# Kernel optimization log

Measured on AMD Instinct MI355X. Metric: run time of the kernel, lower is better.

The kernel has to match this reference:

```python
import jax, jax.numpy as jnp
import numpy as np

B, C, HID, H, W = 32, 256, 128, 32, 32  # batch, input_dim, hidden_dim, grid


def conv1x1(x, Wt, b):
    # 1x1 Conv2d == channel-mixing matmul. x: [B,Cin,H,W], Wt: [Cout,Cin]
    return jnp.einsum('oc,bchw->bohw', Wt, x) + b[None, :, None, None]


def setup_inputs() -> dict:
    key = jax.random.key(0)
    ks = jax.random.split(key, 18)
    p = lambda k, shape: (jax.random.normal(k, shape, jnp.float32) * 0.02)
    return {
        'h': jax.random.normal(ks[0], (B, C, H, W), jnp.float32),
        'm': jax.random.normal(ks[1], (B, C, H, W), jnp.float32),
        'Wq': p(ks[2], (HID, C)),  'bq': p(ks[3], (HID,)),
        'Wk': p(ks[4], (HID, C)),  'bk': p(ks[5], (HID,)),
        'Wv': p(ks[6], (C, C)),    'bv': p(ks[7], (C,)),
        'Wk2': p(ks[8], (HID, C)), 'bk2': p(ks[9], (HID,)),
        'Wv2': p(ks[10], (C, C)),  'bv2': p(ks[11], (C,)),
        'Wz': p(ks[12], (2 * C, 2 * C)), 'bz': p(ks[13], (2 * C,)),
        'Wm': p(ks[14], (3 * C, 3 * C)), 'bm': p(ks[15], (3 * C,)),
    }


def reference(h, m, Wq, bq, Wk, bk, Wv, bv, Wk2, bk2, Wv2, bv2, Wz, bz, Wm, bm):
    Bb, Cc, Hh, Ww = h.shape
    HW = Hh * Ww
    # shared query from h: [B, HID, HW]
    q = conv1x1(h, Wq, bq).reshape(Bb, -1, HW)
    # self-attention branch over h (unscaled logits, as in original)
    kh = conv1x1(h, Wk, bk).reshape(Bb, -1, HW)
    A_h = jax.nn.softmax(jnp.einsum('bdp,bdq->bpq', q, kh), axis=-1)  # [B,HW,HW]
    vh = conv1x1(h, Wv, bv).reshape(Bb, Cc, HW)
    Z_h = jnp.einsum('bpq,bcq->bcp', A_h, vh).reshape(Bb, Cc, Hh, Ww)
    # cross-attention branch over memory m with shared q
    km = conv1x1(m, Wk2, bk2).reshape(Bb, -1, HW)
    A_m = jax.nn.softmax(jnp.einsum('bdp,bdq->bpq', q, km), axis=-1)
    vm = conv1x1(m, Wv2, bv2).reshape(Bb, Cc, HW)
    Z_m = jnp.einsum('bpq,bcq->bcp', A_m, vm).reshape(Bb, Cc, Hh, Ww)
    # fuse, then LSTM-style gating
    Z = conv1x1(jnp.concatenate([Z_h, Z_m], axis=1), Wz, bz)          # [B,2C,H,W]
    comb = conv1x1(jnp.concatenate([Z, h], axis=1), Wm, bm)           # [B,3C,H,W]
    mo, mg, mi = jnp.split(comb, 3, axis=1)
    mi = jax.nn.sigmoid(mi)
    new_m = (1.0 - mi) * m + mi * jnp.tanh(mg)
    new_h = jax.nn.sigmoid(mo) * new_m
    return new_h, new_m
```

## Files before the change

kernel.cpp:

```cpp
#include <hip/hip_runtime.h>
#include <hip/hip_bf16.h>

typedef __bf16  v8bf __attribute__((ext_vector_type(8)));
typedef float   v4f  __attribute__((ext_vector_type(4)));
typedef float   f4   __attribute__((ext_vector_type(4)));
typedef unsigned short us8 __attribute__((ext_vector_type(8)));
typedef unsigned short us4 __attribute__((ext_vector_type(4)));
typedef unsigned int u32;

#define BATCH 32
#define CDIM  256
#define HW    1024

#define OFF_HBT 0L
#define OFF_MBT (OFF_HBT + 16777216L)
#define OFF_QKH (OFF_MBT + 16777216L)
#define OFF_QKM (OFF_QKH + 16777216L)
#define OFF_VH  (OFF_QKM + 8388608L)
#define OFF_VM  (OFF_VH  + 16777216L)
#define OFF_ZCT (OFF_VM  + 16777216L)
#define OFF_W   (OFF_ZCT + 33554432L)
#define OFF_B   (OFF_W   + 3866624L)
#define OFF_CMB OFF_MBT
#define WS_TOTAL (OFF_B + 2944L * 4)
#define W_QK  0
#define W_K2  65536
#define W_V   98304
#define W_V2  163840
#define W_M   491520
#define W_ZT  1081344
#define W_F   1343488
#define B_QK  0
#define B_K2  256
#define B_V   384
#define B_V2  640
#define B_F   2176

__device__ inline unsigned short f2u(float x) {
    __hip_bfloat16 h = __float2bfloat16(x);
    union { __hip_bfloat16 h; unsigned short u; } cv; cv.h = h; return cv.u;
}
__device__ inline float u2f(unsigned short u) {
    union { unsigned short u; __hip_bfloat16 h; } cv; cv.u = u; return __bfloat162float(cv.h);
}
__device__ inline float sigmoidf_(float x) {
    x = fminf(fmaxf(x, -30.f), 30.f);
    return 1.f / (1.f + __expf(-x));
}
__device__ inline float tanhf_(float x) {
    x = fminf(fmaxf(x, -15.f), 15.f);
    float e = __expf(2.f * x);
    return (e - 1.f) / (e + 1.f);
}
__device__ inline void glds16(const unsigned short* g, unsigned short* l) {
    __builtin_amdgcn_global_load_lds(
        (const __attribute__((address_space(1))) u32*)g,
        (__attribute__((address_space(3))) u32*)l, 16, 0, 0);
}

__global__ __launch_bounds__(256)
void prep(const float* __restrict__ hsrc, const float* __restrict__ msrc,
          const float* __restrict__ Wq, const float* __restrict__ Wk,
          const float* __restrict__ Wv, const float* __restrict__ Wk2,
          const float* __restrict__ Wv2, const float* __restrict__ Wz,
          const float* __restrict__ Wm,
          const float* __restrict__ bq, const float* __restrict__ bk,
          const float* __restrict__ bk2, const float* __restrict__ bv,
          const float* __restrict__ bv2, const float* __restrict__ bz,
          const float* __restrict__ bm,
          char* __restrict__ ws)
{
    __shared__ float t[64][68];
    unsigned short* wdst = (unsigned short*)(ws + OFF_W);
    float*          bdst = (float*)(ws + OFF_B);
    const int bid = blockIdx.x;
    const int tid = threadIdx.x;

    if (bid < 6025) {
        const int gid = bid * 256 + tid;
        if (gid < 1081344) {
            const float* s; int off;
            if      (gid <   32768) { s = Wq;  off = gid; }
            else if (gid <   65536) { s = Wk;  off = gid -   32768; }
            else if (gid <   98304) { s = Wk2; off = gid -   65536; }
            else if (gid <  163840) { s = Wv;  off = gid -   98304; }
            else if (gid <  229376) { s = Wv2; off = gid -  163840; }
            else if (gid <  491520) { s = Wz;  off = gid -  229376; }
            else                    { s = Wm;  off = gid -  491520; }
            wdst[gid] = f2u(s[off]);
        } else if (gid < 1343488) {
            const int idx = gid - 1081344;
            const int k = idx >> 9, j = idx & 511;
            wdst[gid] = f2u(Wz[j * 512 + k]);
        } else if (gid < 1540096) {
            const int idx = gid - 1343488;
            const int o = idx >> 8, kk = 512 + (idx & 255);
            wdst[W_F + o * 768 + kk] = f2u(Wm[o * 768 + kk]);
        } else {
            const int bi = gid - 1540096;
            if (bi < 2176) {
                const float* s; int off;
                if      (bi <  128) { s = bq;  off = bi; }
                else if (bi <  256) { s = bk;  off = bi -  128; }
                else if (bi <  384) { s = bk2; off = bi -  256; }
                else if (bi <  640) { s = bv;  off = bi -  384; }
                else if (bi <  896) { s = bv2; off = bi -  640; }
                else if (bi < 1408) { s = bz;  off = bi -  896; }
                else                { s = bm;  off = bi - 1408; }
                bdst[bi] = s[off];
            }
        }
    } else if (bid < 6028) {
        const int o = (bid - 6025) * 256 + tid;
        if (o < 768) {
            float s = bm[o];
            const float* r = Wm + (long)o * 768;
#pragma unroll 8
            for (int j = 0; j < 512; ++j) s += r[j] * bz[j];
            bdst[B_F + o] = s;
        }
    } else {
        const int tz = bid - 6028;
        const int z  = tz >> 6;
        const int p0 = (tz & 15) * 64;
        const int c0 = ((tz >> 4) & 3) * 64;
        const float* src = (z < BATCH) ? hsrc + (long)z * CDIM * HW
                                       : msrc + (long)(z - BATCH) * CDIM * HW;
        unsigned short* dst = (unsigned short*)(ws + ((z < BATCH) ? OFF_HBT : OFF_MBT))
                              + (long)((z < BATCH) ? z : z - BATCH) * HW * CDIM;
        const int r  = tid >> 4;
        const int c4 = (tid & 15) * 4;
#pragma unroll
        for (int i = 0; i < 4; ++i) {
            const f4 v = *reinterpret_cast<const f4*>(src + (long)(c0 + r + 16 * i) * HW + p0 + c4);
            t[r + 16 * i][c4 + 0] = v[0];
            t[r + 16 * i][c4 + 1] = v[1];
            t[r + 16 * i][c4 + 2] = v[2];
            t[r + 16 * i][c4 + 3] = v[3];
        }
        __syncthreads();
#pragma unroll
        for (int i = 0; i < 4; ++i) {
            const int pr = r + 16 * i;
            us4 o;
#pragma unroll
            for (int j = 0; j < 4; ++j) o[j] = f2u(t[c4 + j][pr]);
            *reinterpret_cast<us4*>(dst + (long)(p0 + pr) * CDIM + c0 + c4) = o;
        }
    }
}

__device__ __forceinline__
void gemm_core(const unsigned short* __restrict__ A, int lda,
               const unsigned short* __restrict__ A2, int lda2, int kswitch,
               const unsigned short* __restrict__ Bt, int ldb,
               unsigned short* __restrict__ Cp, int ldc,
               int K, const float* __restrict__ bias, int biasMode,
               int m0, int n0,
               unsigned short* As, unsigned short* Bs)
{
    const int tid  = threadIdx.x;
    const int lane = tid & 63;
    const int w    = tid >> 6;

    v4f acc[4][4];
#pragma unroll
    for (int i = 0; i < 4; ++i)
#pragma unroll
        for (int j = 0; j < 4; ++j) acc[i][j] = v4f{0.f, 0.f, 0.f, 0.f};

    const int wm   = (w >> 1) * 64;
    const int wn   = (w & 1) * 64;
    const int fr   = lane & 15;
    const int g    = lane >> 4;

    const int arow = (w << 3) + (lane >> 3);
    const int acol = (((lane & 7) ^ ((lane >> 3) & 7)) * 8);
    const int lbase = (w << 9);

    for (int k0 = 0; k0 < K; k0 += 64) {
        const unsigned short* Ab; int Al; int Ao;
        if (k0 < kswitch) { Ab = A;  Al = lda;  Ao = k0; }
        else              { Ab = A2; Al = lda2; Ao = k0 - kswitch; }
        const unsigned short* ga = Ab + (long)(m0 + arow) * Al + Ao + acol;
        const unsigned short* gb = Bt + (long)(n0 + arow) * ldb + k0 + acol;
#pragma unroll
        for (int i = 0; i < 4; ++i) {
            glds16(ga + (long)(32 * i) * Al, &As[i * 2048 + lbase]);
            glds16(gb + (long)(32 * i) * ldb, &Bs[i * 2048 + lbase]);
        }
        __syncthreads();
#pragma unroll
        for (int ks = 0; ks < 2; ++ks) {
            const int slot = ((ks * 4 + g) ^ (fr & 7)) * 8;
            v8bf af[4], bfv[4];
#pragma unroll
            for (int mi = 0; mi < 4; ++mi)
                af[mi] = *reinterpret_cast<const v8bf*>(&As[(wm + mi * 16 + fr) * 64 + slot]);
#pragma unroll
            for (int ni = 0; ni < 4; ++ni)
                bfv[ni] = *reinterpret_cast<const v8bf*>(&Bs[(wn + ni * 16 + fr) * 64 + slot]);
#pragma unroll
            for (int mi = 0; mi < 4; ++mi)
#pragma unroll
                for (int ni = 0; ni < 4; ++ni)
                    acc[mi][ni] = __builtin_amdgcn_mfma_f32_16x16x32_bf16(af[mi], bfv[ni], acc[mi][ni], 0, 0, 0);
        }
        __syncthreads();
    }

    const int rbase0 = m0 + wm + g * 4;
#pragma unroll
    for (int mi = 0; mi < 4; ++mi) {
#pragma unroll
        for (int ni = 0; ni < 4; ++ni) {
            const int col = n0 + wn + ni * 16 + fr;
            const int rb  = rbase0 + mi * 16;
            const float bn = (biasMode == 1) ? bias[col] : 0.f;
#pragma unroll
            for (int r = 0; r < 4; ++r) {
                float x = acc[mi][ni][r] + bn;
                if (biasMode == 2) x += bias[rb + r];
                Cp[(long)(rb + r) * ldc + col] = f2u(x);
            }
        }
    }
}

__global__ __launch_bounds__(256)
void gemm_multi(char* __restrict__ ws)
{
    __shared__ unsigned short As[128 * 64];
    __shared__ unsigned short Bs[128 * 64];
    unsigned short* wA = (unsigned short*)(ws + OFF_W);
    float*          bA = (float*)(ws + OFF_B);
    const int id = blockIdx.x;

    if (id < 512) {
        const int b = id >> 4, x = id & 7, y = (id >> 3) & 1;
        const unsigned short* A = (unsigned short*)(ws + OFF_HBT) + (long)b * 262144;
        gemm_core(A, 256, A, 256, 1 << 30, wA + W_QK, 256,
                  (unsigned short*)(ws + OFF_QKH) + (long)b * 262144, 256,
                  256, bA + B_QK, 1, x * 128, y * 128, As, Bs);
    } else if (id < 768) {
        const int idx = id - 512, b = idx >> 3, x = idx & 7;
        const unsigned short* A = (unsigned short*)(ws + OFF_MBT) + (long)b * 262144;
        gemm_core(A, 256, A, 256, 1 << 30, wA + W_K2, 256,
                  (unsigned short*)(ws + OFF_QKM) + (long)b * 131072, 128,
                  256, bA + B_K2, 1, x * 128, 0, As, Bs);
    } else if (id < 1280) {
        const int idx = id - 768, b = idx >> 4, x = idx & 1, y = (idx >> 1) & 7;
        gemm_core(wA + W_V, 256, wA + W_V, 256, 1 << 30,
                  (unsigned short*)(ws + OFF_HBT) + (long)b * 262144, 256,
                  (unsigned short*)(ws + OFF_VH) + (long)b * 262144, 1024,
                  256, bA + B_V, 2, x * 128, y * 128, As, Bs);
    } else if (id < 1792) {
        const int idx = id - 1280, b = idx >> 4, x = idx & 1, y = (idx >> 1) & 7;
        gemm_core(wA + W_V2, 256, wA + W_V2, 256, 1 << 30,
                  (unsigned short*)(ws + OFF_MBT) + (long)b * 262144, 256,
                  (unsigned short*)(ws + OFF_VM) + (long)b * 262144, 1024,
                  256, bA + B_V2, 2, x * 128, y * 128, As, Bs);
    } else {
        const int idx = id - 1792, x = idx % 6, y = idx / 6;
        gemm_core(wA + W_M, 768, wA + W_M, 768, 1 << 30, wA + W_ZT, 512,
                  wA + W_F, 768, 512, bA, 0, x * 128, y * 128, As, Bs);
    }
}

__global__ __launch_bounds__(256)
void gemm_bf16(const unsigned short* __restrict__ A, int lda, long sA,
               const unsigned short* __restrict__ A2, int lda2, long sA2, int kswitch,
               const unsigned short* __restrict__ Bt, int ldb, long sB,
               unsigned short* __restrict__ Cp, int ldc, long sC,
               int K, const float* __restrict__ bias, int biasMode)
{
    __shared__ unsigned short As[128 * 64];
    __shared__ unsigned short Bs[128 * 64];
    const int b = blockIdx.z;
    gemm_core(A + (long)b * sA, lda, A2 + (long)b * sA2, lda2, kswitch,
              Bt + (long)b * sB, ldb, Cp + (long)b * sC, ldc,
              K, bias, biasMode, blockIdx.x * 128, blockIdx.y * 128, As, Bs);
}

__global__ __launch_bounds__(512, 4)
void attn_fused(const unsigned short* __restrict__ Qb, long sQ, int ldq,
                const unsigned short* __restrict__ K0, long sK0, int ldk0,
                const unsigned short* __restrict__ V0,
                const unsigned short* __restrict__ K1, long sK1, int ldk1,
                const unsigned short* __restrict__ V1,
                unsigned short* __restrict__ Out, long sO)
{
    __shared__ unsigned short Qs[64 * 128];
    __shared__ unsigned short Ks[64 * 128];
    __shared__ unsigned short Vs[256 * 64];
    __shared__ unsigned short Ps[64 * 64];

    const int id = blockIdx.x;
    const int c8 = id & 7;
    const int k  = id >> 3;
    const int z  = c8 * 8 + (k >> 4);
    const int p0 = (k & 15) * 64;

    const int b  = (z < 32) ? z : z - 32;
    const unsigned short* Kp; const unsigned short* Vp; int ldk, outoff;
    if (z < 32) { Kp = K0 + (long)b * sK0; Vp = V0 + (long)b * 262144L; ldk = ldk0; outoff = 0; }
    else        { Kp = K1 + (long)b * sK1; Vp = V1 + (long)b * 262144L; ldk = ldk1; outoff = 256; }
    const unsigned short* Qp = Qb + (long)b * sQ;
    Out += (long)b * sO;

    const int tid  = threadIdx.x;
    const int lane = tid & 63;
    const int w    = tid >> 6;
    const int fr   = lane & 15;
    const int g    = lane >> 4;
    const int wp   = w >> 2;
    const int wq   = w & 3;

    v4f vacc[2][4];
#pragma unroll
    for (int i = 0; i < 2; ++i)
#pragma unroll
        for (int j = 0; j < 4; ++j) vacc[i][j] = v4f{0.f, 0.f, 0.f, 0.f};
    float rp[2][4];
#pragma unroll
    for (int i = 0; i < 2; ++i)
#pragma unroll
        for (int r = 0; r < 4; ++r) rp[i][r] = 0.f;

    const int srow   = tid >> 4;
    const int schunk = ((tid & 15) ^ (srow & 7)) * 8;
    const int vrow   = tid >> 3;
    const int vchunk = ((tid & 7) ^ (vrow & 7)) * 8;
    const int sdst   = w * 512;
    const int kr     = wq * 16 + fr;

#define TSWZ(p) (((p) & 7) ^ ((((p) >> 3) & 1) * 3))

#define STAGE_Q()                                                              \
    { _Pragma("unroll")                                                        \
      for (int i = 0; i < 2; ++i)                                              \
          glds16(Qp + (long)(p0 + i * 32 + srow) * ldq + schunk,               \
                 &Qs[i * 4096 + sdst]); }
#define STAGE_K(t)                                                             \
    { const int kv0 = (t) * 64;                                                \
      _Pragma("unroll")                                                        \
      for (int i = 0; i < 2; ++i)                                              \
          glds16(Kp + (long)(kv0 + i * 32 + srow) * ldk + schunk,              \
                 &Ks[i * 4096 + sdst]); }
#define STAGE_V(t)                                                             \
    { const int kv0 = (t) * 64;                                                \
      _Pragma("unroll")                                                        \
      for (int i = 0; i < 4; ++i)                                              \
          glds16(Vp + (long)(i * 64 + vrow) * 1024 + kv0 + vchunk,             \
                 &Vs[i * 4096 + sdst]); }

    STAGE_Q();
    STAGE_K(0);

    for (int t = 0; t < 16; ++t) {
        __syncthreads();
        STAGE_V(t);

        v4f sacc[2];
#pragma unroll
        for (int mi = 0; mi < 2; ++mi) sacc[mi] = v4f{0.f, 0.f, 0.f, 0.f};
        __builtin_amdgcn_s_setprio(1);
#pragma unroll
        for (int ks = 0; ks < 4; ++ks) {
            const v8bf kf = *reinterpret_cast<const v8bf*>(
                &Ks[kr * 128 + ((ks * 4 + g) ^ (kr & 7)) * 8]);
#pragma unroll
            for (int mi = 0; mi < 2; ++mi) {
                const int qrow = wp * 32 + mi * 16 + fr;
                const v8bf qf = *reinterpret_cast<const v8bf*>(
                    &Qs[qrow * 128 + ((ks * 4 + g) ^ (qrow & 7)) * 8]);
                sacc[mi] = __builtin_amdgcn_mfma_f32_16x16x32_bf16(qf, kf, sacc[mi], 0, 0, 0);
            }
        }
        __builtin_amdgcn_s_setprio(0);
#pragma unroll
        for (int mi = 0; mi < 2; ++mi)
#pragma unroll
            for (int r = 0; r < 4; ++r) {
                const float e = __expf(sacc[mi][r]);
                rp[mi][r] += e;
                const int prow = wp * 32 + mi * 16 + g * 4 + r;
                Ps[prow * 64 + (kr ^ (TSWZ(prow) << 3))] = f2u(e);
            }

        __syncthreads();
        if (t < 15) STAGE_K(t + 1);

        __builtin_amdgcn_s_setprio(1);
#pragma unroll
        for (int ks = 0; ks < 2; ++ks) {
            v8bf pf[2], vf[4];
#pragma unroll
            for (int mi = 0; mi < 2; ++mi) {
                const int pr = wp * 32 + mi * 16 + fr;
                pf[mi] = *reinterpret_cast<const v8bf*>(
                    &Ps[pr * 64 + ((ks * 4 + g) ^ TSWZ(pr)) * 8]);
            }
#pragma unroll
            for (int ni = 0; ni < 4; ++ni) {
                const int vr = wq * 64 + ni * 16 + fr;
                vf[ni] = *reinterpret_cast<const v8bf*>(
                    &Vs[vr * 64 + ((ks * 4 + g) ^ (vr & 7)) * 8]);
            }
#pragma unroll
            for (int mi = 0; mi < 2; ++mi)
#pragma unroll
                for (int ni = 0; ni < 4; ++ni)
                    vacc[mi][ni] = __builtin_amdgcn_mfma_f32_16x16x32_bf16(pf[mi], vf[ni], vacc[mi][ni], 0, 0, 0);
        }
        __builtin_amdgcn_s_setprio(0);
    }
#undef STAGE_Q
#undef STAGE_K
#undef STAGE_V
#undef TSWZ

    __syncthreads();
    float* red = reinterpret_cast<float*>(Ps);
#pragma unroll
    for (int mi = 0; mi < 2; ++mi)
#pragma unroll
        for (int r = 0; r < 4; ++r) {
            float v = rp[mi][r];
            v += __shfl_xor(v, 1);
            v += __shfl_xor(v, 2);
            v += __shfl_xor(v, 4);
            v += __shfl_xor(v, 8);
            if (fr == 0) red[wq * 64 + wp * 32 + mi * 16 + g * 4 + r] = v;
        }
    __syncthreads();

#pragma unroll
    for (int mi = 0; mi < 2; ++mi)
#pragma unroll
        for (int r = 0; r < 4; ++r) {
            const int pl = wp * 32 + mi * 16 + g * 4 + r;
            const float inv = 1.f / (red[pl] + red[64 + pl] + red[128 + pl] + red[192 + pl]);
#pragma unroll
            for (int ni = 0; ni < 4; ++ni)
                Out[(long)(p0 + pl) * 512 + outoff + wq * 64 + ni * 16 + fr]
                    = f2u(vacc[mi][ni][r] * inv);
        }
}

__global__ __launch_bounds__(256)
void gating(const unsigned short* __restrict__ combT, const float* __restrict__ m,
            float* __restrict__ outh, float* __restrict__ outm)
{
    const int b  = blockIdx.y;
    const int p0 = blockIdx.x * 32;
    __shared__ unsigned short t[32 * 776];
    const unsigned short* src = combT + ((long)b * HW + p0) * 768;
    const int tid = threadIdx.x;
    for (int i = tid; i < 32 * 96; i += 256) {
        const int rr = i / 96;
        const int cc = (i % 96) * 8;
        *reinterpret_cast<us8*>(&t[rr * 776 + cc]) =
            *reinterpret_cast<const us8*>(src + (long)rr * 768 + cc);
    }
    __syncthreads();
    const int pl = tid & 31;
    const int cl = tid >> 5;
    for (int ci = 0; ci < 32; ++ci) {
        const int c = ci * 8 + cl;
        const float mo = u2f(t[pl * 776 + c]);
        const float mg = u2f(t[pl * 776 + 256 + c]);
        const float mi = u2f(t[pl * 776 + 512 + c]);
        const long gi = ((long)b * CDIM + c) * HW + p0 + pl;
        const float mv = m[gi];
        const float ms = sigmoidf_(mi);
        const float nm = (1.f - ms) * mv + ms * tanhf_(mg);
        const float nh = sigmoidf_(mo) * nm;
        outh[gi] = nh;
        outm[gi] = nm;
    }
}

extern "C" void kernel_launch(void* const* d_in, const int* in_sizes, int n_in,
                              void* d_out, int out_size, void* d_ws, size_t ws_size,
                              hipStream_t stream)
{
    const float* h   = (const float*)d_in[0];
    const float* m   = (const float*)d_in[1];
    const float* Wq  = (const float*)d_in[2];
    const float* bq  = (const float*)d_in[3];
    const float* Wk  = (const float*)d_in[4];
    const float* bk  = (const float*)d_in[5];
    const float* Wv  = (const float*)d_in[6];
    const float* bv  = (const float*)d_in[7];
    const float* Wk2 = (const float*)d_in[8];
    const float* bk2 = (const float*)d_in[9];
    const float* Wv2 = (const float*)d_in[10];
    const float* bv2 = (const float*)d_in[11];
    const float* Wz  = (const float*)d_in[12];
    const float* bz  = (const float*)d_in[13];
    const float* Wm  = (const float*)d_in[14];
    const float* bm  = (const float*)d_in[15];

    char* ws = (char*)d_ws;
    if (ws_size < (size_t)WS_TOTAL) return;

    unsigned short* hT  = (unsigned short*)(ws + OFF_HBT);
    unsigned short* qkh = (unsigned short*)(ws + OFF_QKH);
    unsigned short* qkm = (unsigned short*)(ws + OFF_QKM);
    unsigned short* vh  = (unsigned short*)(ws + OFF_VH);
    unsigned short* vm  = (unsigned short*)(ws + OFF_VM);
    unsigned short* zct = (unsigned short*)(ws + OFF_ZCT);
    unsigned short* cmb = (unsigned short*)(ws + OFF_CMB);
    unsigned short* wA  = (unsigned short*)(ws + OFF_W);
    float*          bA  = (float*)(ws + OFF_B);

    float* outh = (float*)d_out;
    float* outm = outh + 8388608L;

    prep<<<dim3(10124), dim3(256), 0, stream>>>(
        h, m, Wq, Wk, Wv, Wk2, Wv2, Wz, Wm,
        bq, bk, bk2, bv, bv2, bz, bm, ws);

    gemm_multi<<<dim3(1816), dim3(256), 0, stream>>>(ws);

    attn_fused<<<dim3(1024), dim3(512), 0, stream>>>(
        qkh, 262144L, 256,
        qkh + 128, 262144L, 256, vh,
        qkm, 131072L, 128, vm,
        zct, 524288L);

    gemm_bf16<<<dim3(8, 6, 32), dim3(256), 0, stream>>>(
        zct, 512, 524288L, hT, 256, 262144L, 512,
        wA + W_F, 768, 0L, cmb, 768, 786432L, 768, bA + B_F, 1);

    gating<<<dim3(32, 32), dim3(256), 0, stream>>>(cmb, m, outh, outm);
}
```

Baseline: 243.9 us.

## Replace batched comb GEMM with 256x256-tile double-buffered kernel and simplify P swizzle

The final combination GEMM moves from a batched 128x128-tile launch to a flattened-M kernel with 256x256 tiles and 512 threads. It double-buffers LDS stages with explicit vmcnt waits and barriers, and remaps workgroup IDs in an XCD-aware order. The larger tiles are meant to raise operand reuse and overlap loads with MFMA work, at the cost of more LDS and registers and a smaller grid. Separately, the attention kernel's P-tile swizzle is simplified to a plain row XOR, which may change LDS bank conflicts.

```diff
diff --git a/kernel.cpp b/kernel.cpp
--- a/kernel.cpp
+++ b/kernel.cpp
@@ -267,19 +267,107 @@
     }
 }
 
-__global__ __launch_bounds__(256)
-void gemm_bf16(const unsigned short* __restrict__ A, int lda, long sA,
-               const unsigned short* __restrict__ A2, int lda2, long sA2, int kswitch,
-               const unsigned short* __restrict__ Bt, int ldb, long sB,
-               unsigned short* __restrict__ Cp, int ldc, long sC,
-               int K, const float* __restrict__ bias, int biasMode)
+__global__ __launch_bounds__(512, 2)
+void comb_gemm(const unsigned short* __restrict__ A, int lda,
+               const unsigned short* __restrict__ A2, int lda2, int kswitch,
+               const unsigned short* __restrict__ Bt, int ldb,
+               unsigned short* __restrict__ Cp, int ldc,
+               int K, const float* __restrict__ bias, int ntilesN)
 {
-    __shared__ unsigned short As[128 * 64];
-    __shared__ unsigned short Bs[128 * 64];
-    const int b = blockIdx.z;
-    gemm_core(A + (long)b * sA, lda, A2 + (long)b * sA2, lda2, kswitch,
-              Bt + (long)b * sB, ldb, Cp + (long)b * sC, ldc,
-              K, bias, biasMode, blockIdx.x * 128, blockIdx.y * 128, As, Bs);
+    __shared__ unsigned short As[2][256 * 64];
+    __shared__ unsigned short Bs[2][256 * 64];
+
+    const int nwg = gridDim.x;
+    const int wg  = (blockIdx.x & 7) * (nwg >> 3) + (blockIdx.x >> 3);
+    const int m0  = (wg / ntilesN) * 256;
+    const int n0  = (wg % ntilesN) * 256;
+
+    const int tid  = threadIdx.x;
+    const int lane = tid & 63;
+    const int w    = tid >> 6;
+    const int fr   = lane & 15;
+    const int g    = lane >> 4;
+    const int wm   = (w >> 2) * 128;
+    const int wn   = (w & 3) * 64;
+
+    const int srow   = tid >> 3;
+    const int schunk = ((tid & 7) ^ (srow & 7)) * 8;
+    const int sdst   = w * 512;
+
+    v4f acc[8][4];
+#pragma unroll
+    for (int i = 0; i < 8; ++i)
+#pragma unroll
+        for (int j = 0; j < 4; ++j) acc[i][j] = v4f{0.f, 0.f, 0.f, 0.f};
+
+    const int nt = K >> 6;
+
+#define CSTAGE(t, bi)                                                          \
+    { const int k0 = (t) * 64;                                                 \
+      const unsigned short* Ab; int Al; int Ao;                                \
+      if (k0 < kswitch) { Ab = A;  Al = lda;  Ao = k0; }                       \
+      else              { Ab = A2; Al = lda2; Ao = k0 - kswitch; }             \
+      _Pragma("unroll")                                                        \
+      for (int i = 0; i < 4; ++i) {                                            \
+          glds16(Ab + (long)(m0 + i * 64 + srow) * Al + Ao + schunk,           \
+                 &As[bi][i * 4096 + sdst]);                                    \
+          glds16(Bt + (long)(n0 + i * 64 + srow) * ldb + k0 + schunk,          \
+                 &Bs[bi][i * 4096 + sdst]);                                    \
+      } }
+
+    CSTAGE(0, 0);
+    CSTAGE(1, 1);
+
+    for (int t = 0; t < nt; ++t) {
+        if (t + 1 < nt) asm volatile("s_waitcnt vmcnt(8)" ::: "memory");
+        else            asm volatile("s_waitcnt vmcnt(0)" ::: "memory");
+        __builtin_amdgcn_s_barrier();
+        asm volatile("" ::: "memory");
+
+        const unsigned short* Ar = As[t & 1];
+        const unsigned short* Br = Bs[t & 1];
+        __builtin_amdgcn_s_setprio(1);
+#pragma unroll
+        for (int ks = 0; ks < 2; ++ks) {
+            v8bf af[8], bf[4];
+#pragma unroll
+            for (int mi = 0; mi < 8; ++mi) {
+                const int r = wm + mi * 16 + fr;
+                af[mi] = *reinterpret_cast<const v8bf*>(
+                    &Ar[r * 64 + ((ks * 4 + g) ^ (r & 7)) * 8]);
+            }
+#pragma unroll
+            for (int ni = 0; ni < 4; ++ni) {
+                const int r = wn + ni * 16 + fr;
+                bf[ni] = *reinterpret_cast<const v8bf*>(
+                    &Br[r * 64 + ((ks * 4 + g) ^ (r & 7)) * 8]);
+            }
+#pragma unroll
+            for (int mi = 0; mi < 8; ++mi)
+#pragma unroll
+                for (int ni = 0; ni < 4; ++ni)
+                    acc[mi][ni] = __builtin_amdgcn_mfma_f32_16x16x32_bf16(af[mi], bf[ni], acc[mi][ni], 0, 0, 0);
+        }
+        __builtin_amdgcn_s_setprio(0);
+        asm volatile("" ::: "memory");
+        __builtin_amdgcn_s_barrier();
+        if (t + 2 < nt) CSTAGE(t + 2, t & 1);
+    }
+#undef CSTAGE
+
+    const int rbase0 = m0 + wm + g * 4;
+#pragma unroll
+    for (int mi = 0; mi < 8; ++mi) {
+#pragma unroll
+        for (int ni = 0; ni < 4; ++ni) {
+            const int col = n0 + wn + ni * 16 + fr;
+            const int rb  = rbase0 + mi * 16;
+            const float bn = bias[col];
+#pragma unroll
+            for (int r = 0; r < 4; ++r)
+                Cp[(long)(rb + r) * ldc + col] = f2u(acc[mi][ni][r] + bn);
+        }
+    }
 }
 
 __global__ __launch_bounds__(512, 4)
@@ -333,8 +421,6 @@
     const int vchunk = ((tid & 7) ^ (vrow & 7)) * 8;
     const int sdst   = w * 512;
     const int kr     = wq * 16 + fr;
-
-#define TSWZ(p) (((p) & 7) ^ ((((p) >> 3) & 1) * 3))
 
 #define STAGE_Q()                                                              \
     { _Pragma("unroll")                                                        \
@@ -385,7 +471,7 @@
                 const float e = __expf(sacc[mi][r]);
                 rp[mi][r] += e;
                 const int prow = wp * 32 + mi * 16 + g * 4 + r;
-                Ps[prow * 64 + (kr ^ (TSWZ(prow) << 3))] = f2u(e);
+                Ps[prow * 64 + (kr ^ ((prow & 7) << 3))] = f2u(e);
             }
 
         __syncthreads();
@@ -399,7 +485,7 @@
             for (int mi = 0; mi < 2; ++mi) {
                 const int pr = wp * 32 + mi * 16 + fr;
                 pf[mi] = *reinterpret_cast<const v8bf*>(
-                    &Ps[pr * 64 + ((ks * 4 + g) ^ TSWZ(pr)) * 8]);
+                    &Ps[pr * 64 + ((ks * 4 + g) ^ (pr & 7)) * 8]);
             }
 #pragma unroll
             for (int ni = 0; ni < 4; ++ni) {
@@ -418,7 +504,6 @@
 #undef STAGE_Q
 #undef STAGE_K
 #undef STAGE_V
-#undef TSWZ
 
     __syncthreads();
     float* red = reinterpret_cast<float*>(Ps);
@@ -530,9 +615,9 @@
         qkm, 131072L, 128, vm,
         zct, 524288L);
 
-    gemm_bf16<<<dim3(8, 6, 32), dim3(256), 0, stream>>>(
-        zct, 512, 524288L, hT, 256, 262144L, 512,
-        wA + W_F, 768, 0L, cmb, 768, 786432L, 768, bA + B_F, 1);
+    comb_gemm<<<dim3(384), dim3(512), 0, stream>>>(
+        zct, 512, hT, 256, 512,
+        wA + W_F, 768, cmb, 768, 768, bA + B_F, 3);
 
     gating<<<dim3(32, 32), dim3(256), 0, stream>>>(cmb, m, outh, outm);
 }
```

Result: no change. 244.4 us (+0.2%).
